# Optimization experiments

Measured on AMD Instinct MI355X. Metric: run time of the kernel, lower is better.

The kernel has to match this reference:

```python
import jax, jax.numpy as jnp
import numpy as np

NGRAM = 3  # no_repeat_ngram_size from init_kwargs


def setup_inputs() -> dict:
    key = jax.random.key(0)
    k1, k2 = jax.random.split(key)
    bsz, beam_size, step = 32, 8, 511
    R = bsz * beam_size          # 256 hypotheses
    L = step + 1                 # 512 generated tokens so far
    V = 128000                   # vocab size
    # small id range so n-grams actually repeat and bans fire
    tokens = jax.random.randint(k1, (R, L), 0, 100, dtype=jnp.int32)
    lprobs = jax.random.normal(k2, (R, V), dtype=jnp.float32)
    return {"tokens": tokens, "lprobs": lprobs, "bsz": bsz,
            "beam_size": beam_size, "step": step}


def reference(tokens, lprobs, bsz, beam_size, step):
    """Vectorized equivalent of NGramRepeatBlock._no_repeat_ngram.

    For each row, every n-gram in `tokens` whose first n-1 tokens equal the
    current prefix tokens[step+2-n : step+1] contributes its last token to
    the banned set; banned lprobs entries are set to -inf.
    """
    n = NGRAM
    assert tokens.shape[0] == bsz * beam_size
    assert lprobs.shape[0] == bsz * beam_size
    if step + 2 - n < 0:  # static python condition, same as original
        return lprobs
    R, L = tokens.shape
    W = L - n + 1  # number of sliding n-gram windows
    win_idx = jnp.arange(W)[:, None] + jnp.arange(n)[None, :]  # [W, n]
    windows = tokens[:, win_idx]                               # [R, W, n]
    prefix = tokens[:, step + 2 - n: step + 1]                 # [R, n-1]
    # window matches current (n-1)-token prefix -> ban its last token
    match = jnp.all(windows[:, :, : n - 1] == prefix[:, None, :], axis=-1)  # [R, W]
    last = windows[:, :, -1]                                   # [R, W]
    rows = jnp.arange(R)[:, None]
    ban = jnp.zeros(lprobs.shape, dtype=bool).at[rows, last].max(match)  # [R, V]
    return jnp.where(ban, -jnp.inf, lprobs)
```

## Files before the change

### kernel.cpp

```cpp
#include <hip/hip_runtime.h>


#define SENTINEL_BITS 0xFF7F0000u

__global__ void ngram_copy_kernel(const float4* __restrict__ in,
                                  float4* __restrict__ out,
                                  long n4) {
    long i = (long)blockIdx.x * blockDim.x + threadIdx.x;
    long stride = (long)gridDim.x * blockDim.x;
    for (long k = i; k < n4; k += stride) {
        out[k] = in[k];
    }
}

__global__ void ngram_tail_kernel(const float* __restrict__ in,
                                  float* __restrict__ out,
                                  long base, long n) {
    long i = base + (long)blockIdx.x * blockDim.x + threadIdx.x;
    if (i < n) out[i] = in[i];
}

__global__ void ngram_ban_kernel(const int* __restrict__ tokens,
                                 float* __restrict__ out,
                                 const int* __restrict__ step_ptr,
                                 int tokens_count, int lprobs_count) {
    const int n = 3;
    int step = *step_ptr;
    if (step + 2 - n < 0) return;
    int L = step + 1;
    if (L <= 0) return;
    int R = tokens_count / L;
    if (R <= 0) return;
    int V = lprobs_count / R;
    if (V <= 0) return;
    int W = L - n + 1;
    int p_start = step + 2 - n;

    const float sentinel = __uint_as_float(SENTINEL_BITS);

    for (int r = blockIdx.x; r < R; r += gridDim.x) {
        const int* trow = tokens + (size_t)r * L;
        int p0 = trow[p_start];
        int p1 = trow[p_start + 1];
        float* orow = out + (size_t)r * V;
        for (int w = threadIdx.x; w < W; w += blockDim.x) {
            if (trow[w] == p0 && trow[w + 1] == p1) {
                int banned = trow[w + 2];
                if (banned >= 0 && banned < V)
                    orow[banned] = sentinel;
            }
        }
    }
}

extern "C" void kernel_launch(void* const* d_in, const int* in_sizes, int n_in,
                              void* d_out, int out_size, void* d_ws, size_t ws_size,
                              hipStream_t stream) {
    const int*   tokens   = (const int*)d_in[0];
    const float* lprobs   = (const float*)d_in[1];
    const int*   step_ptr = (const int*)d_in[4];
    float*       out      = (float*)d_out;

    long n    = (long)out_size;
    long n4   = n / 4;
    long base = n4 * 4;

    int  threads = 256;
    long blocks  = (n4 + threads - 1) / threads;
    if (blocks > 65535) blocks = 65535;
    if (blocks < 1)     blocks = 1;

    ngram_copy_kernel<<<(int)blocks, threads, 0, stream>>>(
        (const float4*)lprobs, (float4*)out, n4);

    if (n - base > 0) {
        ngram_tail_kernel<<<1, 256, 0, stream>>>(lprobs, out, base, n);
    }

    int ban_blocks = 256;
    ngram_ban_kernel<<<ban_blocks, 256, 0, stream>>>(
        tokens, out, step_ptr, in_sizes[0], in_sizes[1]);
}
```

Before: 230.9 us.

## Fuse lprobs copy and n-gram ban into one chunked kernel

Replaces the separate copy, tail and ban kernels with a single kernel. Each block copies a 16K-element chunk of a row using nontemporal vector loads and stores, then scans that row's tokens and writes bans that fall inside its chunk. This removes extra launches and the serialized ban pass. In exchange, each row's token scan is repeated once per chunk, about eight times per row.

```diff
diff --git a/kernel.cpp b/kernel.cpp
--- a/kernel.cpp
+++ b/kernel.cpp
@@ -2,52 +2,73 @@
 
 
 #define SENTINEL_BITS 0xFF7F0000u
+#define CHUNK_ELEMS   16384
+#define NGRAM_N       3
 
-__global__ void ngram_copy_kernel(const float4* __restrict__ in,
-                                  float4* __restrict__ out,
-                                  long n4) {
-    long i = (long)blockIdx.x * blockDim.x + threadIdx.x;
-    long stride = (long)gridDim.x * blockDim.x;
-    for (long k = i; k < n4; k += stride) {
-        out[k] = in[k];
+typedef float f32x4 __attribute__((ext_vector_type(4)));
+
+__global__ __launch_bounds__(256)
+void ngram_fused_kernel(const int* __restrict__ tokens,
+                        const float* __restrict__ lprobs,
+                        float* __restrict__ out,
+                        const int* __restrict__ step_ptr,
+                        int tokens_count, int lprobs_count)
+{
+    const int step = *step_ptr;
+    const int L = step + 1;
+    const int R = (L > 0) ? (tokens_count / L) : 0;
+    const int V = (R > 0) ? (lprobs_count / R) : 0;
+
+    if (R <= 0 || V <= 0) {
+        long nTot = lprobs_count;
+        long stride = (long)gridDim.x * blockDim.x;
+        for (long k = (long)blockIdx.x * blockDim.x + threadIdx.x;
+             k < nTot; k += stride)
+            out[k] = lprobs[k];
+        return;
     }
-}
 
-__global__ void ngram_tail_kernel(const float* __restrict__ in,
-                                  float* __restrict__ out,
-                                  long base, long n) {
-    long i = base + (long)blockIdx.x * blockDim.x + threadIdx.x;
-    if (i < n) out[i] = in[i];
-}
+    const bool do_ban  = (step + 2 - NGRAM_N) >= 0;
+    const int  W       = L - NGRAM_N + 1;
+    const int  p_start = step + 2 - NGRAM_N;
+    const float sentinel = __uint_as_float(SENTINEL_BITS);
+    const bool vec_ok = ((V & 3) == 0);
 
-__global__ void ngram_ban_kernel(const int* __restrict__ tokens,
-                                 float* __restrict__ out,
-                                 const int* __restrict__ step_ptr,
-                                 int tokens_count, int lprobs_count) {
-    const int n = 3;
-    int step = *step_ptr;
-    if (step + 2 - n < 0) return;
-    int L = step + 1;
-    if (L <= 0) return;
-    int R = tokens_count / L;
-    if (R <= 0) return;
-    int V = lprobs_count / R;
-    if (V <= 0) return;
-    int W = L - n + 1;
-    int p_start = step + 2 - n;
+    const int  chunks_per_row = (V + CHUNK_ELEMS - 1) / CHUNK_ELEMS;
+    const long total_chunks   = (long)R * chunks_per_row;
 
-    const float sentinel = __uint_as_float(SENTINEL_BITS);
+    for (long c = blockIdx.x; c < total_chunks; c += gridDim.x) {
+        const int r  = (int)(c / chunks_per_row);
+        const int ci = (int)(c % chunks_per_row);
+        const int e0 = ci * CHUNK_ELEMS;
+        const int e1 = min(e0 + CHUNK_ELEMS, V);
+        const size_t rbase = (size_t)r * V;
 
-    for (int r = blockIdx.x; r < R; r += gridDim.x) {
-        const int* trow = tokens + (size_t)r * L;
-        int p0 = trow[p_start];
-        int p1 = trow[p_start + 1];
-        float* orow = out + (size_t)r * V;
-        for (int w = threadIdx.x; w < W; w += blockDim.x) {
-            if (trow[w] == p0 && trow[w + 1] == p1) {
-                int banned = trow[w + 2];
-                if (banned >= 0 && banned < V)
-                    orow[banned] = sentinel;
+        if (vec_ok) {
+            const f32x4* in4  = (const f32x4*)(lprobs + rbase);
+            f32x4*       out4 = (f32x4*)(out + rbase);
+            const int f0 = e0 >> 2;
+            const int f1 = e1 >> 2;
+            for (int k = f0 + (int)threadIdx.x; k < f1; k += blockDim.x) {
+                f32x4 v = __builtin_nontemporal_load(in4 + k);
+                __builtin_nontemporal_store(v, out4 + k);
+            }
+        } else {
+            for (int e = e0 + (int)threadIdx.x; e < e1; e += blockDim.x)
+                out[rbase + e] = lprobs[rbase + e];
+        }
+
+        if (do_ban && W > 0) {
+            __syncthreads();
+            const int* trow = tokens + (size_t)r * L;
+            const int p0 = trow[p_start];
+            const int p1 = trow[p_start + 1];
+            for (int w = (int)threadIdx.x; w < W; w += blockDim.x) {
+                if (trow[w] == p0 && trow[w + 1] == p1) {
+                    const int banned = trow[w + 2];
+                    if (banned >= e0 && banned < e1)
+                        out[rbase + banned] = sentinel;
+                }
             }
         }
     }
@@ -61,23 +82,12 @@
     const int*   step_ptr = (const int*)d_in[4];
     float*       out      = (float*)d_out;
 
-    long n    = (long)out_size;
-    long n4   = n / 4;
-    long base = n4 * 4;
+    const int threads = 256;
+    int blocks = 2048;
+    long est_chunks = ((long)out_size + CHUNK_ELEMS - 1) / CHUNK_ELEMS + 256;
+    if (est_chunks < blocks) blocks = (int)est_chunks;
+    if (blocks < 1) blocks = 1;
 
-    int  threads = 256;
-    long blocks  = (n4 + threads - 1) / threads;
-    if (blocks > 65535) blocks = 65535;
-    if (blocks < 1)     blocks = 1;
-
-    ngram_copy_kernel<<<(int)blocks, threads, 0, stream>>>(
-        (const float4*)lprobs, (float4*)out, n4);
-
-    if (n - base > 0) {
-        ngram_tail_kernel<<<1, 256, 0, stream>>>(lprobs, out, base, n);
-    }
-
-    int ban_blocks = 256;
-    ngram_ban_kernel<<<ban_blocks, 256, 0, stream>>>(
-        tokens, out, step_ptr, in_sizes[0], in_sizes[1]);
+    ngram_fused_kernel<<<blocks, threads, 0, stream>>>(
+        tokens, lprobs, out, step_ptr, in_sizes[0], in_sizes[1]);
 }
```

After: 235.1 us. No clear change (+1.8%).
